# Optimization experiments

Hardware: AMD Instinct MI355X
Metric: run time of the kernel (lower is better)

The kernel has to match this reference:

```python
import jax, jax.numpy as jnp
from jax import lax
import numpy as np

B, N, C = 16, 4096, 64
RATIO = 0.25
M = int(N * RATIO)      # 1024 sampled centers
R = 0.2                 # radius
K = 64                  # max_num_neighbors
H = 128                 # MLP hidden/out width
NEG = -1e30


def setup_inputs() -> dict:
    key = jax.random.key(0)
    k1, k2, k3, k4 = jax.random.split(key, 4)
    pos = jax.random.uniform(k1, (B, N, 3), dtype=jnp.float32)
    x = jax.random.normal(k2, (B, N, C), dtype=jnp.float32)
    W1 = jax.random.normal(k3, (C + 3, H), dtype=jnp.float32) / np.sqrt(C + 3)
    b1 = jnp.zeros((H,), jnp.float32)
    W2 = jax.random.normal(k4, (H, H), dtype=jnp.float32) / np.sqrt(H)
    b2 = jnp.zeros((H,), jnp.float32)
    return {"x": x, "pos": pos, "W1": W1, "b1": b1, "W2": W2, "b2": b2}


def _fps_single(p, m):
    """Farthest point sampling on one cloud p:[N,3] -> m int32 indices (start at 0)."""
    n = p.shape[0]
    big = jnp.full((n,), jnp.finfo(p.dtype).max, dtype=p.dtype)

    def step(carry, _):
        dists, last = carry
        d = jnp.sum((p - p[last]) ** 2, axis=-1)       # [N]
        dists = jnp.minimum(dists, d)
        nxt = jnp.argmax(dists).astype(jnp.int32)
        return (dists, nxt), nxt

    (_, _), idxs = lax.scan(step, (big, jnp.int32(0)), None, length=m - 1)
    return jnp.concatenate([jnp.zeros((1,), jnp.int32), idxs])


def reference(x, pos, W1, b1, W2, b2):
    # --- FPS: sample M centers per cloud ---
    idx = jax.vmap(lambda p: _fps_single(p, M))(pos)                 # [B,M] int32
    pos_s = jax.vmap(lambda p, i: p[i])(pos, idx)                    # [B,M,3]

    # --- radius ball query: pairwise sq-dists via |a|^2+|b|^2-2ab (no [B,M,N,3]) ---
    pn = jnp.sum(pos * pos, axis=-1)                                 # [B,N]
    sn = jnp.sum(pos_s * pos_s, axis=-1)                             # [B,M]
    d2 = sn[:, :, None] + pn[:, None, :] - 2.0 * jnp.einsum("bmc,bnc->bmn", pos_s, pos)
    mask = d2 <= R * R                                               # [B,M,N]

    # first K in-radius neighbors by index (torch_cluster-style capped neighbor list)
    ar = jnp.arange(N, dtype=jnp.int32)
    scored = jnp.where(mask, -ar[None, None, :], -N)                 # valid -> -idx
    vals, _ = lax.top_k(scored, K)                                   # [B,M,K]
    nbr = -vals                                                      # neighbor indices, N = invalid
    valid = nbr < N                                                  # [B,M,K]
    nbr_c = jnp.minimum(nbr, N - 1)

    # --- gather -> MLP -> masked max aggregation (PointConv, aggr='max') ---
    x_j = jax.vmap(lambda xb, ib: xb[ib])(x, nbr_c)                  # [B,M,K,C]
    pos_j = jax.vmap(lambda pb, ib: pb[ib])(pos, nbr_c)              # [B,M,K,3]
    feat = jnp.concatenate([x_j, pos_j - pos_s[:, :, None, :]], axis=-1)  # [B,M,K,C+3]

    h = jax.nn.relu(jnp.einsum("bmkc,ch->bmkh", feat, W1) + b1)
    h = jax.nn.relu(jnp.einsum("bmkh,hg->bmkg", h, W2) + b2)          # [B,M,K,H]

    h = jnp.where(valid[..., None], h, NEG)
    out = jnp.max(h, axis=2)                                          # [B,M,H]
    out = jnp.where(jnp.any(valid, axis=2)[..., None], out, 0.0)
    return out, pos_s
```

## Files before the change

kernel.cpp:

```cpp
#include <hip/hip_runtime.h>
#include <cstdint>
#include <cstddef>

#define BB 16
#define NN 4096
#define CC 64
#define MM 1024
#define KK 64
#define HH 128
#define NEGV -1.0e30f

#define FTH 256
#define FPT 16
#define NPROD 16
#define GTOT 256
#define PSTRIDE 32

#define KC1 96
#define SA 104
#define SH 136
#define HSTRIDE 41984

typedef __attribute__((ext_vector_type(8))) short bf16x8;
typedef __attribute__((ext_vector_type(4))) float f32x4;
typedef __attribute__((ext_vector_type(2))) float f32x2;

__device__ __forceinline__ unsigned int f2bf(float f) {
  unsigned int u = __float_as_uint(f);
  return (u + 0x7fffu + ((u >> 16) & 1u)) >> 16;
}
__device__ __forceinline__ void split2(float f, unsigned int& h, unsigned int& l) {
  h = f2bf(f);
  float hf = __uint_as_float(h << 16);
  l = f2bf(f - hf);
}

template <int CTRL, int RM>
__device__ __forceinline__ void dpp_max64(unsigned int& hi, unsigned int& lo) {
  unsigned int shi = (unsigned int)__builtin_amdgcn_update_dpp(
      (int)hi, (int)hi, CTRL, RM, 0xf, false);
  unsigned int slo = (unsigned int)__builtin_amdgcn_update_dpp(
      (int)lo, (int)lo, CTRL, RM, 0xf, false);
  unsigned long long cur = ((unsigned long long)hi << 32) | lo;
  unsigned long long oth = ((unsigned long long)shi << 32) | slo;
  if (oth > cur) { hi = shi; lo = slo; }
}

__global__ __launch_bounds__(128) void wprep_kernel(
    const float* __restrict__ W1, const float* __restrict__ W2,
    unsigned short* __restrict__ W1Th, unsigned short* __restrict__ W1Tl,
    unsigned short* __restrict__ W2Th, unsigned short* __restrict__ W2Tl,
    unsigned int* __restrict__ progress, unsigned int* __restrict__ claim) {
  const int n = blockIdx.x, t = threadIdx.x;
  if (n == 0) {
    for (int j = t; j < NPROD * PSTRIDE; j += 128) progress[j] = 0u;
    if (t == 0) *claim = 0u;
  }
  if (t < KC1) {
    float v = (t < 67) ? W1[(size_t)t * HH + n] : 0.0f;
    unsigned int h, l; split2(v, h, l);
    W1Th[n * KC1 + t] = (unsigned short)h;
    W1Tl[n * KC1 + t] = (unsigned short)l;
  }
  {
    float v = W2[(size_t)t * HH + n];
    unsigned int h, l; split2(v, h, l);
    W2Th[n * HH + t] = (unsigned short)h;
    W2Tl[n * HH + t] = (unsigned short)l;
  }
}

__global__ __launch_bounds__(512, 2) void fused_kernel(
    const float* __restrict__ pos, const float* __restrict__ x,
    float* __restrict__ pos_s_ws, float* __restrict__ pos_s_out,
    const unsigned short* __restrict__ W1Th, const unsigned short* __restrict__ W1Tl,
    const unsigned short* __restrict__ W2Th, const unsigned short* __restrict__ W2Tl,
    const float* __restrict__ b1, const float* __restrict__ b2,
    float* __restrict__ out,
    unsigned int* __restrict__ progress, unsigned int* __restrict__ claim) {
#pragma clang fp contract(off)
  __shared__ __attribute__((aligned(16))) unsigned char LBUF[83968];
  const int t = threadIdx.x;
  const int lane = t & 63;

  if (blockIdx.x < NPROD) {
    if (t >= FTH) return;
    __builtin_amdgcn_s_setprio(3);
    const int wv = t >> 6;
    const int b = blockIdx.x;
    float4* P4 = (float4*)LBUF;
    float* SXa = (float*)(LBUF + 65536);
    float* SYa = (float*)(LBUF + 69632);
    float* SZa = (float*)(LBUF + 73728);
    unsigned long long* cand = (unsigned long long*)(LBUF + 77824);
    const float* pb = pos + (size_t)b * NN * 3;
    f32x2 px[8], py[8], pz[8], dd[8];
#pragma unroll
    for (int j = 0; j < FPT; ++j) {
      int i = t + j * FTH;
      float xx = pb[i * 3 + 0], yy = pb[i * 3 + 1], zz = pb[i * 3 + 2];
      P4[i] = make_float4(xx, yy, zz, 0.0f);
      px[j >> 1][j & 1] = xx;
      py[j >> 1][j & 1] = yy;
      pz[j >> 1][j & 1] = zz;
      dd[j >> 1][j & 1] = 3.4028234663852886e38f;
    }
    __syncthreads();
    float4 c4 = P4[0];
    float sx = c4.x, sy = c4.y, sz = c4.z;
    if (t == 0) { SXa[0] = sx; SYa[0] = sy; SZa[0] = sz; }

    for (int m = 1; m < MM; ++m) {
      f32x2 s2x = {sx, sx}, s2y = {sy, sy}, s2z = {sz, sz};
      float nv[16];
#pragma unroll
      for (int k = 0; k < 8; ++k) {
        f32x2 dx = px[k] - s2x, dy = py[k] - s2y, dz = pz[k] - s2z;
        f32x2 d2 = (dx * dx + dy * dy) + dz * dz;
        float n0 = fminf(dd[k][0], d2[0]);
        float n1 = fminf(dd[k][1], d2[1]);
        dd[k][0] = n0;
        dd[k][1] = n1;
        nv[2 * k] = n0;
        nv[2 * k + 1] = n1;
      }
      float tv[8]; int ti[8];
#pragma unroll
      for (int k = 0; k < 8; ++k) {
        bool c = nv[2 * k + 1] > nv[2 * k];
        tv[k] = c ? nv[2 * k + 1] : nv[2 * k];
        ti[k] = c ? (2 * k + 1) : (2 * k);
      }
      float uv[4]; int ui[4];
#pragma unroll
      for (int k = 0; k < 4; ++k) {
        bool c = tv[2 * k + 1] > tv[2 * k];
        uv[k] = c ? tv[2 * k + 1] : tv[2 * k];
        ui[k] = c ? ti[2 * k + 1] : ti[2 * k];
      }
      float wv2[2]; int wi2[2];
#pragma unroll
      for (int k = 0; k < 2; ++k) {
        bool c = uv[2 * k + 1] > uv[2 * k];
        wv2[k] = c ? uv[2 * k + 1] : uv[2 * k];
        wi2[k] = c ? ui[2 * k + 1] : ui[2 * k];
      }
      bool cf = wv2[1] > wv2[0];
      float bv = cf ? wv2[1] : wv2[0];
      int bj = cf ? wi2[1] : wi2[0];
      int bi = t + (bj << 8);

      unsigned int kh = __float_as_uint(bv);
      unsigned int kl = ~(unsigned int)bi;
      dpp_max64<0x111, 0xf>(kh, kl);
      dpp_max64<0x112, 0xf>(kh, kl);
      dpp_max64<0x114, 0xf>(kh, kl);
      dpp_max64<0x118, 0xf>(kh, kl);
      dpp_max64<0x142, 0xa>(kh, kl);
      dpp_max64<0x143, 0xc>(kh, kl);
      if (lane == 63)
        cand[(m & 1) * 4 + wv] = ((unsigned long long)kh << 32) | kl;
      __syncthreads();
      unsigned long long best = cand[(m & 1) * 4 + 0];
#pragma unroll
      for (int w = 1; w < 4; ++w) {
        unsigned long long ok = cand[(m & 1) * 4 + w];
        best = ok > best ? ok : best;
      }
      int fi = (int)(~(unsigned int)(best & 0xffffffffull));
      float4 w4 = P4[fi];
      sx = w4.x; sy = w4.y; sz = w4.z;
      if (t == 0) { SXa[m] = sx; SYa[m] = sy; SZa[m] = sz; }
      if ((m & 15) == 15) {
        if (t < 16) {
          int idx = (m - 15) + t;
          float fx = SXa[idx], fy = SYa[idx], fz = SZa[idx];
          size_t o = ((size_t)b * MM + idx) * 3;
          __hip_atomic_store(&pos_s_ws[o + 0], fx, __ATOMIC_RELAXED, __HIP_MEMORY_SCOPE_AGENT);
          __hip_atomic_store(&pos_s_ws[o + 1], fy, __ATOMIC_RELAXED, __HIP_MEMORY_SCOPE_AGENT);
          __hip_atomic_store(&pos_s_ws[o + 2], fz, __ATOMIC_RELAXED, __HIP_MEMORY_SCOPE_AGENT);
        }
      } else if ((m & 15) == 0 && t == 0) {
        asm volatile("s_waitcnt vmcnt(0)" ::: "memory");
        __hip_atomic_store(&progress[b * PSTRIDE], (unsigned int)m,
                           __ATOMIC_RELAXED, __HIP_MEMORY_SCOPE_AGENT);
      }
    }
    __syncthreads();
    if (t == 0) {
      asm volatile("s_waitcnt vmcnt(0)" ::: "memory");
      __hip_atomic_store(&progress[b * PSTRIDE], (unsigned int)MM,
                         __ATOMIC_RELAXED, __HIP_MEMORY_SCOPE_AGENT);
    }
    for (int i = t; i < MM; i += FTH) {
      size_t o = ((size_t)b * MM + i) * 3;
      pos_s_out[o + 0] = SXa[i];
      pos_s_out[o + 1] = SYa[i];
      pos_s_out[o + 2] = SZa[i];
    }
    return;
  }

  const int h = t >> 8;
  const int th = t & 255;
  const int wvh = (t >> 6) & 3;
  unsigned char* HB = LBUF + h * HSTRIDE;
  unsigned short* Ah = (unsigned short*)HB;
  unsigned short* Al = (unsigned short*)(HB + 64 * SA * 2);
  unsigned short* Hh = (unsigned short*)HB;
  unsigned short* Hl = (unsigned short*)(HB + 64 * SH * 2);
  int* nbr_s = (int*)(HB + 34816);
  unsigned long long* masksL = (unsigned long long*)(HB + 35072);
  int* prefixL = (int*)(HB + 35584);
  float* ctr = (float*)(HB + 35840);
  int* cntS = (int*)(HB + 35856);
  volatile int* cidShare = (int*)(LBUF + 83960);
  const int r = lane & 15, q = lane >> 4;
  const int wbase = wvh * 32;

  while (true) {
    if (t == 0) {
      unsigned int i = __hip_atomic_fetch_add(claim, 2u, __ATOMIC_RELAXED,
                                              __HIP_MEMORY_SCOPE_AGENT);
      *cidShare = (int)i;
    }
    __syncthreads();
    int i0 = *cidShare;
    if (i0 >= BB * MM) break;
    const int i = i0 + h;
    const bool active = (i < BB * MM);
    const int cid = active ? (((i & 15) << 10) | (i >> 4)) : 0;
    const int b = cid >> 10;
    const int m = cid & 1023;

    if (active && th < 64) {
      while ((int)__hip_atomic_load(&progress[b * PSTRIDE], __ATOMIC_RELAXED,
                                    __HIP_MEMORY_SCOPE_AGENT) <= m)
        __builtin_amdgcn_s_sleep(64);
    }
    if (active && th < 3)
      ctr[th] = __hip_atomic_load(&pos_s_ws[(size_t)cid * 3 + th],
                                  __ATOMIC_RELAXED, __HIP_MEMORY_SCOPE_AGENT);
    __syncthreads();

    const float sx = ctr[0], sy = ctr[1], sz = ctr[2];
    const float sn = (sx * sx + sy * sy) + sz * sz;
    const float* pb = pos + (size_t)b * NN * 3;
    if (active) {
#pragma unroll
      for (int cc = 0; cc < 16; ++cc) {
        int c = (wvh << 4) + cc;
        int n = (c << 6) + lane;
        float xx = pb[n * 3 + 0], yy = pb[n * 3 + 1], zz = pb[n * 3 + 2];
        float pnn = (xx * xx + yy * yy) + zz * zz;
        float dot = __builtin_fmaf(sz, zz, __builtin_fmaf(sy, yy, sx * xx));
        float d2 = (sn + pnn) - 2.0f * dot;
        bool pred = d2 <= 0.04f;
        unsigned long long mask = __ballot(pred);
        if (lane == 0) masksL[c] = mask;
      }
    }
    __syncthreads();
    if (active && th < 64) {
      int pc = (int)__popcll(masksL[lane]);
      int incl = pc;
#pragma unroll
      for (int off = 1; off < 64; off <<= 1) {
        int o2 = __shfl_up(incl, off, 64);
        if (lane >= off) incl += o2;
      }
      prefixL[lane] = incl - pc;
      if (lane == 63) *cntS = incl < KK ? incl : KK;
    }
    __syncthreads();
    const int cnt = *cntS;
    if (active) {
#pragma unroll
      for (int cc = 0; cc < 16; ++cc) {
        int c = (wvh << 4) + cc;
        unsigned long long mk = masksL[c];
        bool pred = (mk >> lane) & 1ull;
        int slot = prefixL[c] + (int)__popcll(mk & ((1ull << lane) - 1ull));
        if (pred && slot < KK) nbr_s[slot] = (c << 6) + lane;
      }
    }
    __syncthreads();

    if (active) {
      const int kn = th >> 2, p = th & 3;
      float vals[16];
      float d0 = 0.0f, d1 = 0.0f, d2v = 0.0f;
      if (kn < cnt) {
        int n = nbr_s[kn];
        const float* xp = x + ((size_t)b * NN + n) * CC + p * 16;
#pragma unroll
        for (int ii = 0; ii < 4; ++ii) {
          float4 v = ((const float4*)xp)[ii];
          vals[ii * 4 + 0] = v.x; vals[ii * 4 + 1] = v.y;
          vals[ii * 4 + 2] = v.z; vals[ii * 4 + 3] = v.w;
        }
        if (p == 0) {
          const float* pp = pos + ((size_t)b * NN + n) * 3;
          d0 = pp[0] - sx; d1 = pp[1] - sy; d2v = pp[2] - sz;
        }
      } else {
#pragma unroll
        for (int ii = 0; ii < 16; ++ii) vals[ii] = 0.0f;
      }
#pragma unroll
      for (int j = 0; j < 16; j += 2) {
        unsigned int h0, l0, h1, l1;
        split2(vals[j], h0, l0);
        split2(vals[j + 1], h1, l1);
        int c = p * 16 + j;
        *(unsigned int*)&Ah[kn * SA + c] = h0 | (h1 << 16);
        *(unsigned int*)&Al[kn * SA + c] = l0 | (l1 << 16);
      }
      if (p == 0) {
        unsigned int h0, l0, h1, l1, h2, l2;
        split2(d0, h0, l0); split2(d1, h1, l1); split2(d2v, h2, l2);
        *(unsigned int*)&Ah[kn * SA + 64] = h0 | (h1 << 16);
        *(unsigned int*)&Al[kn * SA + 64] = l0 | (l1 << 16);
        *(unsigned int*)&Ah[kn * SA + 66] = h2;
        *(unsigned int*)&Al[kn * SA + 66] = l2;
      } else if (p == 1) {
#pragma unroll
        for (int c = 68; c < 80; c += 2) {
          *(unsigned int*)&Ah[kn * SA + c] = 0u;
          *(unsigned int*)&Al[kn * SA + c] = 0u;
        }
      } else if (p == 2) {
#pragma unroll
        for (int c = 80; c < 96; c += 2) {
          *(unsigned int*)&Ah[kn * SA + c] = 0u;
          *(unsigned int*)&Al[kn * SA + c] = 0u;
        }
      }
    }
    __syncthreads();

    f32x4 acc[4][2];
#pragma unroll
    for (int mt = 0; mt < 4; ++mt)
#pragma unroll
      for (int nt = 0; nt < 2; ++nt) acc[mt][nt] = (f32x4)0.0f;

    if (active) {
#pragma unroll
      for (int kc = 0; kc < 3; ++kc) {
        bf16x8 bh[2], bl[2];
#pragma unroll
        for (int nt = 0; nt < 2; ++nt) {
          int o = (wbase + nt * 16 + r) * KC1 + kc * 32 + q * 8;
          bh[nt] = *(const bf16x8*)(W1Th + o);
          bl[nt] = *(const bf16x8*)(W1Tl + o);
        }
#pragma unroll
        for (int mt = 0; mt < 4; ++mt) {
          int o = (mt * 16 + r) * SA + kc * 32 + q * 8;
          bf16x8 ah = *(const bf16x8*)&Ah[o];
          bf16x8 al = *(const bf16x8*)&Al[o];
#pragma unroll
          for (int nt = 0; nt < 2; ++nt) {
            acc[mt][nt] = __builtin_amdgcn_mfma_f32_16x16x32_bf16(ah, bh[nt], acc[mt][nt], 0, 0, 0);
            acc[mt][nt] = __builtin_amdgcn_mfma_f32_16x16x32_bf16(al, bh[nt], acc[mt][nt], 0, 0, 0);
            acc[mt][nt] = __builtin_amdgcn_mfma_f32_16x16x32_bf16(ah, bl[nt], acc[mt][nt], 0, 0, 0);
          }
        }
      }
    }
    __syncthreads();

    if (active) {
      float b1v[2] = { b1[wbase + r], b1[wbase + 16 + r] };
#pragma unroll
      for (int mt = 0; mt < 4; ++mt)
#pragma unroll
        for (int nt = 0; nt < 2; ++nt)
#pragma unroll
          for (int ii = 0; ii < 4; ++ii) {
            int mm = mt * 16 + q * 4 + ii;
            int n = wbase + nt * 16 + r;
            float v = fmaxf(acc[mt][nt][ii] + b1v[nt], 0.0f);
            unsigned int hh2, ll2; split2(v, hh2, ll2);
            Hh[mm * SH + n] = (unsigned short)hh2;
            Hl[mm * SH + n] = (unsigned short)ll2;
          }
    }
    __syncthreads();

#pragma unroll
    for (int mt = 0; mt < 4; ++mt)
#pragma unroll
      for (int nt = 0; nt < 2; ++nt) acc[mt][nt] = (f32x4)0.0f;
    if (active) {
#pragma unroll
      for (int kc = 0; kc < 4; ++kc) {
        bf16x8 bh[2], bl[2];
#pragma unroll
        for (int nt = 0; nt < 2; ++nt) {
          int o = (wbase + nt * 16 + r) * HH + kc * 32 + q * 8;
          bh[nt] = *(const bf16x8*)(W2Th + o);
          bl[nt] = *(const bf16x8*)(W2Tl + o);
        }
#pragma unroll
        for (int mt = 0; mt < 4; ++mt) {
          int o = (mt * 16 + r) * SH + kc * 32 + q * 8;
          bf16x8 ah = *(const bf16x8*)&Hh[o];
          bf16x8 al = *(const bf16x8*)&Hl[o];
#pragma unroll
          for (int nt = 0; nt < 2; ++nt) {
            acc[mt][nt] = __builtin_amdgcn_mfma_f32_16x16x32_bf16(ah, bh[nt], acc[mt][nt], 0, 0, 0);
            acc[mt][nt] = __builtin_amdgcn_mfma_f32_16x16x32_bf16(al, bh[nt], acc[mt][nt], 0, 0, 0);
            acc[mt][nt] = __builtin_amdgcn_mfma_f32_16x16x32_bf16(ah, bl[nt], acc[mt][nt], 0, 0, 0);
          }
        }
      }
      float b2v[2] = { b2[wbase + r], b2[wbase + 16 + r] };
#pragma unroll
      for (int nt = 0; nt < 2; ++nt) {
        float vmax = NEGV;
#pragma unroll
        for (int mt = 0; mt < 4; ++mt)
#pragma unroll
          for (int ii = 0; ii < 4; ++ii) {
            int mm = mt * 16 + q * 4 + ii;
            float v = fmaxf(acc[mt][nt][ii] + b2v[nt], 0.0f);
            if (mm < cnt) vmax = fmaxf(vmax, v);
          }
        vmax = fmaxf(vmax, __shfl_xor(vmax, 16, 64));
        vmax = fmaxf(vmax, __shfl_xor(vmax, 32, 64));
        if (q == 0)
          out[(size_t)cid * HH + wbase + nt * 16 + r] = (cnt > 0) ? vmax : 0.0f;
      }
    }
    __syncthreads();
  }
}

extern "C" void kernel_launch(void* const* d_in, const int* in_sizes, int n_in,
                              void* d_out, int out_size, void* d_ws, size_t ws_size,
                              hipStream_t stream) {
  const float* x   = (const float*)d_in[0];
  const float* pos = (const float*)d_in[1];
  const float* W1  = (const float*)d_in[2];
  const float* b1  = (const float*)d_in[3];
  const float* W2  = (const float*)d_in[4];
  const float* b2  = (const float*)d_in[5];
  float* out = (float*)d_out;
  float* pos_s_out = out + (size_t)BB * MM * HH;

  char* ws = (char*)d_ws;
  float* pos_s_ws = (float*)(ws);
  unsigned short* W1Th = (unsigned short*)(ws + 458752);
  unsigned short* W1Tl = (unsigned short*)(ws + 483328);
  unsigned short* W2Th = (unsigned short*)(ws + 507904);
  unsigned short* W2Tl = (unsigned short*)(ws + 540672);
  unsigned int* progress = (unsigned int*)(ws + 573440);
  unsigned int* claim    = (unsigned int*)(ws + 575488);

  wprep_kernel<<<HH, 128, 0, stream>>>(W1, W2, W1Th, W1Tl, W2Th, W2Tl,
                                       progress, claim);
  fused_kernel<<<GTOT, 512, 0, stream>>>(pos, x, pos_s_ws, pos_s_out,
                                         W1Th, W1Tl, W2Th, W2Tl, b1, b2, out,
                                         progress, claim);
}
```

Measured before the change: 767.5 us.

## Process two FPS batches per producer block to interleave independent chains

Each FPS producer block now runs farthest-point sampling for two point clouds at once, interleaving their distance updates, tournament reductions and DPP max reductions so the two independent dependency chains can hide each other's latency, and sharing one barrier per iteration. The number of producer blocks halves from 16 to 8, which frees CUs for the consumer MLP blocks. In exchange, register pressure per thread doubles, and LDS grows to about 152KB, which may cut consumer-block occupancy since every block reserves the full shared buffer.

Result: slower. 1.543 ms (+101.0%).

```diff
diff --git a/kernel.cpp b/kernel.cpp
--- a/kernel.cpp
+++ b/kernel.cpp
@@ -12,7 +12,8 @@
 
 #define FTH 256
 #define FPT 16
-#define NPROD 16
+#define NPRODB 8
+#define BATCHES 16
 #define GTOT 256
 #define PSTRIDE 32
 
@@ -20,6 +21,8 @@
 #define SA 104
 #define SH 136
 #define HSTRIDE 41984
+
+#define LBUF_SZ 155776
 
 typedef __attribute__((ext_vector_type(8))) short bf16x8;
 typedef __attribute__((ext_vector_type(4))) float f32x4;
@@ -46,6 +49,33 @@
   if (oth > cur) { hi = shi; lo = slo; }
 }
 
+__device__ __forceinline__ void tourn16(const float* nv, float& bv, int& bj) {
+  float tv[8]; int ti[8];
+#pragma unroll
+  for (int k = 0; k < 8; ++k) {
+    bool c = nv[2 * k + 1] > nv[2 * k];
+    tv[k] = c ? nv[2 * k + 1] : nv[2 * k];
+    ti[k] = c ? (2 * k + 1) : (2 * k);
+  }
+  float uv[4]; int ui[4];
+#pragma unroll
+  for (int k = 0; k < 4; ++k) {
+    bool c = tv[2 * k + 1] > tv[2 * k];
+    uv[k] = c ? tv[2 * k + 1] : tv[2 * k];
+    ui[k] = c ? ti[2 * k + 1] : ti[2 * k];
+  }
+  float wv2[2]; int wi2[2];
+#pragma unroll
+  for (int k = 0; k < 2; ++k) {
+    bool c = uv[2 * k + 1] > uv[2 * k];
+    wv2[k] = c ? uv[2 * k + 1] : uv[2 * k];
+    wi2[k] = c ? ui[2 * k + 1] : ui[2 * k];
+  }
+  bool cf = wv2[1] > wv2[0];
+  bv = cf ? wv2[1] : wv2[0];
+  bj = cf ? wi2[1] : wi2[0];
+}
+
 __global__ __launch_bounds__(128) void wprep_kernel(
     const float* __restrict__ W1, const float* __restrict__ W2,
     unsigned short* __restrict__ W1Th, unsigned short* __restrict__ W1Tl,
@@ -53,7 +83,7 @@
     unsigned int* __restrict__ progress, unsigned int* __restrict__ claim) {
   const int n = blockIdx.x, t = threadIdx.x;
   if (n == 0) {
-    for (int j = t; j < NPROD * PSTRIDE; j += 128) progress[j] = 0u;
+    for (int j = t; j < BATCHES * PSTRIDE; j += 128) progress[j] = 0u;
     if (t == 0) *claim = 0u;
   }
   if (t < KC1) {
@@ -79,124 +109,158 @@
     float* __restrict__ out,
     unsigned int* __restrict__ progress, unsigned int* __restrict__ claim) {
 #pragma clang fp contract(off)
-  __shared__ __attribute__((aligned(16))) unsigned char LBUF[83968];
+  __shared__ __attribute__((aligned(16))) unsigned char LBUF[LBUF_SZ];
   const int t = threadIdx.x;
   const int lane = t & 63;
 
-  if (blockIdx.x < NPROD) {
+  if (blockIdx.x < NPRODB) {
     if (t >= FTH) return;
     __builtin_amdgcn_s_setprio(3);
     const int wv = t >> 6;
-    const int b = blockIdx.x;
-    float4* P4 = (float4*)LBUF;
-    float* SXa = (float*)(LBUF + 65536);
-    float* SYa = (float*)(LBUF + 69632);
-    float* SZa = (float*)(LBUF + 73728);
-    unsigned long long* cand = (unsigned long long*)(LBUF + 77824);
-    const float* pb = pos + (size_t)b * NN * 3;
-    f32x2 px[8], py[8], pz[8], dd[8];
+    const int bA = blockIdx.x * 2, bB = bA + 1;
+    float4* P4A = (float4*)LBUF;
+    float4* P4B = (float4*)(LBUF + 65536);
+    float* SXA = (float*)(LBUF + 131072);
+    float* SYA = (float*)(LBUF + 135168);
+    float* SZA = (float*)(LBUF + 139264);
+    float* SXB = (float*)(LBUF + 143360);
+    float* SYB = (float*)(LBUF + 147456);
+    float* SZB = (float*)(LBUF + 151552);
+    unsigned long long* candA = (unsigned long long*)(LBUF + 155648);
+    unsigned long long* candB = (unsigned long long*)(LBUF + 155712);
+    const float* pbA = pos + (size_t)bA * NN * 3;
+    const float* pbB = pos + (size_t)bB * NN * 3;
+    f32x2 pxA[8], pyA[8], pzA[8], ddA[8];
+    f32x2 pxB[8], pyB[8], pzB[8], ddB[8];
 #pragma unroll
     for (int j = 0; j < FPT; ++j) {
       int i = t + j * FTH;
-      float xx = pb[i * 3 + 0], yy = pb[i * 3 + 1], zz = pb[i * 3 + 2];
-      P4[i] = make_float4(xx, yy, zz, 0.0f);
-      px[j >> 1][j & 1] = xx;
-      py[j >> 1][j & 1] = yy;
-      pz[j >> 1][j & 1] = zz;
-      dd[j >> 1][j & 1] = 3.4028234663852886e38f;
-    }
-    __syncthreads();
-    float4 c4 = P4[0];
-    float sx = c4.x, sy = c4.y, sz = c4.z;
-    if (t == 0) { SXa[0] = sx; SYa[0] = sy; SZa[0] = sz; }
+      float ax = pbA[i * 3 + 0], ay = pbA[i * 3 + 1], az = pbA[i * 3 + 2];
+      P4A[i] = make_float4(ax, ay, az, 0.0f);
+      pxA[j >> 1][j & 1] = ax; pyA[j >> 1][j & 1] = ay; pzA[j >> 1][j & 1] = az;
+      ddA[j >> 1][j & 1] = 3.4028234663852886e38f;
+      float bx = pbB[i * 3 + 0], by = pbB[i * 3 + 1], bz = pbB[i * 3 + 2];
+      P4B[i] = make_float4(bx, by, bz, 0.0f);
+      pxB[j >> 1][j & 1] = bx; pyB[j >> 1][j & 1] = by; pzB[j >> 1][j & 1] = bz;
+      ddB[j >> 1][j & 1] = 3.4028234663852886e38f;
+    }
+    __syncthreads();
+    float4 cA = P4A[0];
+    float sxA = cA.x, syA = cA.y, szA = cA.z;
+    float4 cB = P4B[0];
+    float sxB = cB.x, syB = cB.y, szB = cB.z;
+    if (t == 0)  { SXA[0] = sxA; SYA[0] = syA; SZA[0] = szA; }
+    if (t == 64) { SXB[0] = sxB; SYB[0] = syB; SZB[0] = szB; }
 
     for (int m = 1; m < MM; ++m) {
-      f32x2 s2x = {sx, sx}, s2y = {sy, sy}, s2z = {sz, sz};
-      float nv[16];
+      f32x2 sAx = {sxA, sxA}, sAy = {syA, syA}, sAz = {szA, szA};
+      f32x2 sBx = {sxB, sxB}, sBy = {syB, syB}, sBz = {szB, szB};
+      float nvA[16], nvB[16];
 #pragma unroll
       for (int k = 0; k < 8; ++k) {
-        f32x2 dx = px[k] - s2x, dy = py[k] - s2y, dz = pz[k] - s2z;
-        f32x2 d2 = (dx * dx + dy * dy) + dz * dz;
-        float n0 = fminf(dd[k][0], d2[0]);
-        float n1 = fminf(dd[k][1], d2[1]);
-        dd[k][0] = n0;
-        dd[k][1] = n1;
-        nv[2 * k] = n0;
-        nv[2 * k + 1] = n1;
-      }
-      float tv[8]; int ti[8];
-#pragma unroll
-      for (int k = 0; k < 8; ++k) {
-        bool c = nv[2 * k + 1] > nv[2 * k];
-        tv[k] = c ? nv[2 * k + 1] : nv[2 * k];
-        ti[k] = c ? (2 * k + 1) : (2 * k);
-      }
-      float uv[4]; int ui[4];
-#pragma unroll
-      for (int k = 0; k < 4; ++k) {
-        bool c = tv[2 * k + 1] > tv[2 * k];
-        uv[k] = c ? tv[2 * k + 1] : tv[2 * k];
-        ui[k] = c ? ti[2 * k + 1] : ti[2 * k];
-      }
-      float wv2[2]; int wi2[2];
-#pragma unroll
-      for (int k = 0; k < 2; ++k) {
-        bool c = uv[2 * k + 1] > uv[2 * k];
-        wv2[k] = c ? uv[2 * k + 1] : uv[2 * k];
-        wi2[k] = c ? ui[2 * k + 1] : ui[2 * k];
-      }
-      bool cf = wv2[1] > wv2[0];
-      float bv = cf ? wv2[1] : wv2[0];
-      int bj = cf ? wi2[1] : wi2[0];
-      int bi = t + (bj << 8);
-
-      unsigned int kh = __float_as_uint(bv);
-      unsigned int kl = ~(unsigned int)bi;
-      dpp_max64<0x111, 0xf>(kh, kl);
-      dpp_max64<0x112, 0xf>(kh, kl);
-      dpp_max64<0x114, 0xf>(kh, kl);
-      dpp_max64<0x118, 0xf>(kh, kl);
-      dpp_max64<0x142, 0xa>(kh, kl);
-      dpp_max64<0x143, 0xc>(kh, kl);
-      if (lane == 63)
-        cand[(m & 1) * 4 + wv] = ((unsigned long long)kh << 32) | kl;
+        {
+          f32x2 dx = pxA[k] - sAx, dy = pyA[k] - sAy, dz = pzA[k] - sAz;
+          f32x2 d2 = (dx * dx + dy * dy) + dz * dz;
+          float n0 = fminf(ddA[k][0], d2[0]);
+          float n1 = fminf(ddA[k][1], d2[1]);
+          ddA[k][0] = n0; ddA[k][1] = n1;
+          nvA[2 * k] = n0; nvA[2 * k + 1] = n1;
+        }
+        {
+          f32x2 dx = pxB[k] - sBx, dy = pyB[k] - sBy, dz = pzB[k] - sBz;
+          f32x2 d2 = (dx * dx + dy * dy) + dz * dz;
+          float n0 = fminf(ddB[k][0], d2[0]);
+          float n1 = fminf(ddB[k][1], d2[1]);
+          ddB[k][0] = n0; ddB[k][1] = n1;
+          nvB[2 * k] = n0; nvB[2 * k + 1] = n1;
+        }
+      }
+      float bvA, bvB; int bjA, bjB;
+      tourn16(nvA, bvA, bjA);
+      tourn16(nvB, bvB, bjB);
+      int biA = t + (bjA << 8);
+      int biB = t + (bjB << 8);
+
+      unsigned int khA = __float_as_uint(bvA), klA = ~(unsigned int)biA;
+      unsigned int khB = __float_as_uint(bvB), klB = ~(unsigned int)biB;
+      dpp_max64<0x111, 0xf>(khA, klA); dpp_max64<0x111, 0xf>(khB, klB);
+      dpp_max64<0x112, 0xf>(khA, klA); dpp_max64<0x112, 0xf>(khB, klB);
+      dpp_max64<0x114, 0xf>(khA, klA); dpp_max64<0x114, 0xf>(khB, klB);
+      dpp_max64<0x118, 0xf>(khA, klA); dpp_max64<0x118, 0xf>(khB, klB);
+      dpp_max64<0x142, 0xa>(khA, klA); dpp_max64<0x142, 0xa>(khB, klB);
+      dpp_max64<0x143, 0xc>(khA, klA); dpp_max64<0x143, 0xc>(khB, klB);
+      const int p4 = (m & 1) * 4;
+      if (lane == 63) {
+        candA[p4 + wv] = ((unsigned long long)khA << 32) | klA;
+        candB[p4 + wv] = ((unsigned long long)khB << 32) | klB;
+      }
       __syncthreads();
-      unsigned long long best = cand[(m & 1) * 4 + 0];
+      unsigned long long bestA = candA[p4 + 0];
+      unsigned long long bestB = candB[p4 + 0];
 #pragma unroll
       for (int w = 1; w < 4; ++w) {
-        unsigned long long ok = cand[(m & 1) * 4 + w];
-        best = ok > best ? ok : best;
-      }
-      int fi = (int)(~(unsigned int)(best & 0xffffffffull));
-      float4 w4 = P4[fi];
-      sx = w4.x; sy = w4.y; sz = w4.z;
-      if (t == 0) { SXa[m] = sx; SYa[m] = sy; SZa[m] = sz; }
+        unsigned long long oA = candA[p4 + w];
+        unsigned long long oB = candB[p4 + w];
+        bestA = oA > bestA ? oA : bestA;
+        bestB = oB > bestB ? oB : bestB;
+      }
+      int fiA = (int)(~(unsigned int)(bestA & 0xffffffffull));
+      int fiB = (int)(~(unsigned int)(bestB & 0xffffffffull));
+      float4 wA = P4A[fiA];
+      float4 wB = P4B[fiB];
+      sxA = wA.x; syA = wA.y; szA = wA.z;
+      sxB = wB.x; syB = wB.y; szB = wB.z;
+      if (t == 0)  { SXA[m] = sxA; SYA[m] = syA; SZA[m] = szA; }
+      if (t == 64) { SXB[m] = sxB; SYB[m] = syB; SZB[m] = szB; }
       if ((m & 15) == 15) {
         if (t < 16) {
           int idx = (m - 15) + t;
-          float fx = SXa[idx], fy = SYa[idx], fz = SZa[idx];
-          size_t o = ((size_t)b * MM + idx) * 3;
+          float fx = SXA[idx], fy = SYA[idx], fz = SZA[idx];
+          size_t o = ((size_t)bA * MM + idx) * 3;
           __hip_atomic_store(&pos_s_ws[o + 0], fx, __ATOMIC_RELAXED, __HIP_MEMORY_SCOPE_AGENT);
           __hip_atomic_store(&pos_s_ws[o + 1], fy, __ATOMIC_RELAXED, __HIP_MEMORY_SCOPE_AGENT);
           __hip_atomic_store(&pos_s_ws[o + 2], fz, __ATOMIC_RELAXED, __HIP_MEMORY_SCOPE_AGENT);
-        }
-      } else if ((m & 15) == 0 && t == 0) {
-        asm volatile("s_waitcnt vmcnt(0)" ::: "memory");
-        __hip_atomic_store(&progress[b * PSTRIDE], (unsigned int)m,
-                           __ATOMIC_RELAXED, __HIP_MEMORY_SCOPE_AGENT);
+        } else if (t >= 64 && t < 80) {
+          int idx = (m - 15) + (t - 64);
+          float fx = SXB[idx], fy = SYB[idx], fz = SZB[idx];
+          size_t o = ((size_t)bB * MM + idx) * 3;
+          __hip_atomic_store(&pos_s_ws[o + 0], fx, __ATOMIC_RELAXED, __HIP_MEMORY_SCOPE_AGENT);
+          __hip_atomic_store(&pos_s_ws[o + 1], fy, __ATOMIC_RELAXED, __HIP_MEMORY_SCOPE_AGENT);
+          __hip_atomic_store(&pos_s_ws[o + 2], fz, __ATOMIC_RELAXED, __HIP_MEMORY_SCOPE_AGENT);
+        }
+      } else if ((m & 15) == 0) {
+        if (t == 0) {
+          asm volatile("s_waitcnt vmcnt(0)" ::: "memory");
+          __hip_atomic_store(&progress[bA * PSTRIDE], (unsigned int)m,
+                             __ATOMIC_RELAXED, __HIP_MEMORY_SCOPE_AGENT);
+        }
+        if (t == 64) {
+          asm volatile("s_waitcnt vmcnt(0)" ::: "memory");
+          __hip_atomic_store(&progress[bB * PSTRIDE], (unsigned int)m,
+                             __ATOMIC_RELAXED, __HIP_MEMORY_SCOPE_AGENT);
+        }
       }
     }
     __syncthreads();
     if (t == 0) {
       asm volatile("s_waitcnt vmcnt(0)" ::: "memory");
-      __hip_atomic_store(&progress[b * PSTRIDE], (unsigned int)MM,
+      __hip_atomic_store(&progress[bA * PSTRIDE], (unsigned int)MM,
                          __ATOMIC_RELAXED, __HIP_MEMORY_SCOPE_AGENT);
     }
+    if (t == 64) {
+      asm volatile("s_waitcnt vmcnt(0)" ::: "memory");
+      __hip_atomic_store(&progress[bB * PSTRIDE], (unsigned int)MM,
+                         __ATOMIC_RELAXED, __HIP_MEMORY_SCOPE_AGENT);
+    }
     for (int i = t; i < MM; i += FTH) {
-      size_t o = ((size_t)b * MM + i) * 3;
-      pos_s_out[o + 0] = SXa[i];
-      pos_s_out[o + 1] = SYa[i];
-      pos_s_out[o + 2] = SZa[i];
+      size_t oA = ((size_t)bA * MM + i) * 3;
+      pos_s_out[oA + 0] = SXA[i];
+      pos_s_out[oA + 1] = SYA[i];
+      pos_s_out[oA + 2] = SZA[i];
+      size_t oB = ((size_t)bB * MM + i) * 3;
+      pos_s_out[oB + 0] = SXB[i];
+      pos_s_out[oB + 1] = SYB[i];
+      pos_s_out[oB + 2] = SZB[i];
     }
     return;
   }
```

## Use contiguous point ownership and float-only DPP max with ballot argmax in FPS

Applied to the files above, without the earlier changes.

Each FPS thread now owns 16 contiguous points, loaded as vectorized float4 reads, instead of strided points, and the in-thread argmax is fused into the distance loop. The cross-lane reduction does a 32-bit float max via DPP, then recovers the winning lane with a ballot and readlane, replacing the 64-bit packed (value, index) DPP compare. A raw s_barrier and vector LDS reads of the candidates replace __syncthreads and scalar reads. This shortens the serial per-iteration critical path of FPS, but tie-breaking now takes the lowest lane within a wave, and it must still match first-index semantics given the new index mapping.

Result: faster. 751.3 us, median of 2 (-2.1%).

```diff
diff --git a/kernel.cpp b/kernel.cpp
--- a/kernel.cpp
+++ b/kernel.cpp
@@ -36,14 +36,10 @@
 }
 
 template <int CTRL, int RM>
-__device__ __forceinline__ void dpp_max64(unsigned int& hi, unsigned int& lo) {
-  unsigned int shi = (unsigned int)__builtin_amdgcn_update_dpp(
-      (int)hi, (int)hi, CTRL, RM, 0xf, false);
-  unsigned int slo = (unsigned int)__builtin_amdgcn_update_dpp(
-      (int)lo, (int)lo, CTRL, RM, 0xf, false);
-  unsigned long long cur = ((unsigned long long)hi << 32) | lo;
-  unsigned long long oth = ((unsigned long long)shi << 32) | slo;
-  if (oth > cur) { hi = shi; lo = slo; }
+__device__ __forceinline__ float dppmaxf(float v) {
+  int s = __builtin_amdgcn_update_dpp(__float_as_int(v), __float_as_int(v),
+                                      CTRL, RM, 0xf, false);
+  return fmaxf(v, __int_as_float(s));
 }
 
 __global__ __launch_bounds__(128) void wprep_kernel(
@@ -94,16 +90,26 @@
     float* SZa = (float*)(LBUF + 73728);
     unsigned long long* cand = (unsigned long long*)(LBUF + 77824);
     const float* pb = pos + (size_t)b * NN * 3;
-    f32x2 px[8], py[8], pz[8], dd[8];
+
 #pragma unroll
     for (int j = 0; j < FPT; ++j) {
       int i = t + j * FTH;
-      float xx = pb[i * 3 + 0], yy = pb[i * 3 + 1], zz = pb[i * 3 + 2];
-      P4[i] = make_float4(xx, yy, zz, 0.0f);
-      px[j >> 1][j & 1] = xx;
-      py[j >> 1][j & 1] = yy;
-      pz[j >> 1][j & 1] = zz;
-      dd[j >> 1][j & 1] = 3.4028234663852886e38f;
+      P4[i] = make_float4(pb[i * 3 + 0], pb[i * 3 + 1], pb[i * 3 + 2], 0.0f);
+    }
+    f32x2 px[8], py[8], pz[8], dd[8];
+    {
+      const float4* pc4 = (const float4*)(pb + (size_t)t * 48);
+      float4 f4[12];
+#pragma unroll
+      for (int ii = 0; ii < 12; ++ii) f4[ii] = pc4[ii];
+      const float* ff = (const float*)f4;
+#pragma unroll
+      for (int l = 0; l < 16; ++l) {
+        px[l >> 1][l & 1] = ff[l * 3 + 0];
+        py[l >> 1][l & 1] = ff[l * 3 + 1];
+        pz[l >> 1][l & 1] = ff[l * 3 + 2];
+        dd[l >> 1][l & 1] = 3.4028234663852886e38f;
+      }
     }
     __syncthreads();
     float4 c4 = P4[0];
@@ -112,7 +118,7 @@
 
     for (int m = 1; m < MM; ++m) {
       f32x2 s2x = {sx, sx}, s2y = {sy, sy}, s2z = {sz, sz};
-      float nv[16];
+      float tv[8]; int ti[8];
 #pragma unroll
       for (int k = 0; k < 8; ++k) {
         f32x2 dx = px[k] - s2x, dy = py[k] - s2y, dz = pz[k] - s2z;
@@ -121,14 +127,8 @@
         float n1 = fminf(dd[k][1], d2[1]);
         dd[k][0] = n0;
         dd[k][1] = n1;
-        nv[2 * k] = n0;
-        nv[2 * k + 1] = n1;
-      }
-      float tv[8]; int ti[8];
-#pragma unroll
-      for (int k = 0; k < 8; ++k) {
-        bool c = nv[2 * k + 1] > nv[2 * k];
-        tv[k] = c ? nv[2 * k + 1] : nv[2 * k];
+        bool c = n1 > n0;
+        tv[k] = c ? n1 : n0;
         ti[k] = c ? (2 * k + 1) : (2 * k);
       }
       float uv[4]; int ui[4];
@@ -148,25 +148,37 @@
       bool cf = wv2[1] > wv2[0];
       float bv = cf ? wv2[1] : wv2[0];
       int bj = cf ? wi2[1] : wi2[0];
-      int bi = t + (bj << 8);
-
-      unsigned int kh = __float_as_uint(bv);
-      unsigned int kl = ~(unsigned int)bi;
-      dpp_max64<0x111, 0xf>(kh, kl);
-      dpp_max64<0x112, 0xf>(kh, kl);
-      dpp_max64<0x114, 0xf>(kh, kl);
-      dpp_max64<0x118, 0xf>(kh, kl);
-      dpp_max64<0x142, 0xa>(kh, kl);
-      dpp_max64<0x143, 0xc>(kh, kl);
-      if (lane == 63)
-        cand[(m & 1) * 4 + wv] = ((unsigned long long)kh << 32) | kl;
-      __syncthreads();
-      unsigned long long best = cand[(m & 1) * 4 + 0];
-#pragma unroll
-      for (int w = 1; w < 4; ++w) {
-        unsigned long long ok = cand[(m & 1) * 4 + w];
-        best = ok > best ? ok : best;
-      }
+      int bi = t * 16 + bj;
+
+      float mx = bv;
+      mx = dppmaxf<0x111, 0xf>(mx);
+      mx = dppmaxf<0x112, 0xf>(mx);
+      mx = dppmaxf<0x114, 0xf>(mx);
+      mx = dppmaxf<0x118, 0xf>(mx);
+      mx = dppmaxf<0x142, 0xa>(mx);
+      mx = dppmaxf<0x143, 0xc>(mx);
+      float wavemax = __int_as_float(
+          __builtin_amdgcn_readlane(__float_as_int(mx), 63));
+      unsigned long long ball = __ballot(bv == wavemax);
+      int wl = (int)__builtin_ctzll(ball);
+      int wbi = __builtin_amdgcn_readlane(bi, wl);
+
+      const int p4 = (m & 1) * 4;
+      if (lane == 63) {
+        unsigned long long key =
+            ((unsigned long long)__float_as_uint(wavemax) << 32) |
+            (unsigned long long)(~(unsigned int)wbi);
+        cand[p4 + wv] = key;
+      }
+      asm volatile("s_waitcnt lgkmcnt(0)" ::: "memory");
+      __builtin_amdgcn_s_barrier();
+      asm volatile("" ::: "memory");
+
+      ulonglong2 cA = *(const ulonglong2*)(cand + p4);
+      ulonglong2 cB = *(const ulonglong2*)(cand + p4 + 2);
+      unsigned long long m01 = cA.x > cA.y ? cA.x : cA.y;
+      unsigned long long m23 = cB.x > cB.y ? cB.x : cB.y;
+      unsigned long long best = m01 > m23 ? m01 : m23;
       int fi = (int)(~(unsigned int)(best & 0xffffffffull));
       float4 w4 = P4[fi];
       sx = w4.x; sy = w4.y; sz = w4.z;
```
